# Optimization experiments

Hardware: AMD Instinct MI355X
Metric: run time of the kernel (lower is better)

The kernel has to match this reference:

```python
import jax, jax.numpy as jnp
import numpy as np

N_NODES = 100000
N_EDGES = 1600000
DIM = 64
NUM_HEADS = 4
HEAD_DIM = DIM // NUM_HEADS
QK_SCALE = HEAD_DIM ** -0.5
EPS = 1e-16  # matches torch_geometric softmax denominator eps


def setup_inputs() -> dict:
    key = jax.random.key(0)
    k1, k2, k3 = jax.random.split(key, 3)
    x = jax.random.normal(k1, (N_NODES, DIM), dtype=jnp.float32)
    W_qkv = jax.random.normal(k2, (DIM, 3 * DIM), dtype=jnp.float32) * (DIM ** -0.5)
    b_qkv = jnp.zeros((3 * DIM,), dtype=jnp.float32)
    edge_index = jax.random.randint(k3, (2, N_EDGES), 0, N_NODES, dtype=jnp.int64)
    return {"x": x, "W_qkv": W_qkv, "b_qkv": b_qkv, "edge_index": edge_index}


def reference(x, W_qkv, b_qkv, edge_index):
    N = x.shape[0]
    E = edge_index.shape[1]
    # qkv projection: (N, 3, H, d)
    qkv = (x @ W_qkv + b_qkv).reshape(N, 3, NUM_HEADS, HEAD_DIM)
    s = edge_index[0]  # query (source) node per edge
    t = edge_index[1]  # key/value (target) node per edge
    q = qkv[s, 0] * QK_SCALE  # (E, H, d)
    k = qkv[t, 1]             # (E, H, d)
    v = qkv[t, 2]             # (E, H, d)
    compat = jnp.einsum('ehd,ehd->eh', q, k)  # (E, H)
    # segment softmax keyed by source node (numerically stable)
    m = jax.ops.segment_max(compat, s, num_segments=N)          # (N, H)
    ex = jnp.exp(compat - m[s])                                  # (E, H)
    den = jax.ops.segment_sum(ex, s, num_segments=N)             # (N, H)
    attn = ex / (den[s] + EPS)                                   # (E, H)
    # weighted values, flatten heads, scatter-sum back to source nodes
    msg = (v * attn[..., None]).reshape(E, DIM)                  # (E, dim)
    out = jax.ops.segment_sum(msg, s, num_segments=N)            # (N, dim)
    return out
```

## Files before the change

kernel.cpp:

```cpp
#include <hip/hip_runtime.h>

constexpr int N_NODES = 100000;
constexpr int N_EDGES = 1600000;
constexpr int DIM = 64;
constexpr float QK_SCALE = 0.25f;
constexpr float LOG2E = 1.4426950408889634f;
constexpr float EPS = 1e-16f;

constexpr int NBK = (N_NODES + 255) / 256;
constexpr int BCAP = 8192;
constexpr int SC_CHUNK = 8192;
constexpr int SC_BLOCKS = (N_EDGES + SC_CHUNK - 1) / SC_CHUNK;
constexpr int QK_BLOCKS = (N_NODES + 127) / 128;

typedef __attribute__((ext_vector_type(8))) short short8;
typedef __attribute__((ext_vector_type(4))) float f32x4;

__device__ __forceinline__ unsigned short f32_to_bf16_rne(float f) {
    unsigned int u = __float_as_uint(f);
    u += 0x7fffu + ((u >> 16) & 1u);
    return (unsigned short)(u >> 16);
}
__device__ __forceinline__ float bf_lo(unsigned int u) { return __uint_as_float(u << 16); }
__device__ __forceinline__ float bf_hi(unsigned int u) { return __uint_as_float(u & 0xffff0000u); }

__device__ __forceinline__ float qsum4(float p) {
    int a = __builtin_amdgcn_update_dpp(0, __float_as_int(p), 0xB1, 0xF, 0xF, true);
    p += __int_as_float(a);
    int c = __builtin_amdgcn_update_dpp(0, __float_as_int(p), 0x4E, 0xF, 0xF, true);
    p += __int_as_float(c);
    return p;
}

__device__ __forceinline__ int orig_col(int jp) {
    if (jp < 64) return jp;
    const int p = jp - 64;
    const int chunk = p >> 3, w = p & 7;
    return (w < 4) ? (64 + chunk * 4 + w) : (128 + chunk * 4 + (w - 4));
}

__global__ __launch_bounds__(192) void prep_w(const float* __restrict__ W,
                                              const float* __restrict__ b,
                                              unsigned short* __restrict__ Wbt,
                                              float* __restrict__ bb,
                                              int* __restrict__ bcnt) {
    const int jp = threadIdx.x;
    const int k = blockIdx.x;
    const int oc = orig_col(jp);
    const float sc = (jp < 64) ? QK_SCALE * LOG2E : 1.f;
    Wbt[jp * DIM + k] = f32_to_bf16_rne(W[k * 192 + oc] * sc);
    if (k == 0) {
        bb[jp] = b[oc] * sc;
        for (int i = jp; i < NBK; i += 192) bcnt[i] = 0;
    }
}

__global__ __launch_bounds__(512) void proj_scatter(const float* __restrict__ x,
                                                    const unsigned short* __restrict__ Wbt,
                                                    const float* __restrict__ bb,
                                                    unsigned short* __restrict__ qkv_t,
                                                    const int* __restrict__ ei,
                                                    int* __restrict__ bcnt,
                                                    unsigned int* __restrict__ bbuf) {
    __shared__ int h[NBK];
    __shared__ int lofs[NBK];
    __shared__ int gbase[NBK];
    __shared__ int wsum[8];
    __shared__ unsigned int stage[SC_CHUNK];

    if (blockIdx.x < SC_BLOCKS) {
        const int tid = threadIdx.x;
        const int lane = tid & 63;
        const int wid = tid >> 6;
        const int e0 = blockIdx.x * SC_CHUNK;
        const int n = min(SC_CHUNK, N_EDGES - e0);

        for (int i = tid; i < NBK; i += 512) h[i] = 0;
        __syncthreads();

        for (int i = tid; i < n; i += 512)
            atomicAdd(&h[ei[e0 + i] >> 8], 1);
        __syncthreads();

        const int v = (tid < NBK) ? h[tid] : 0;
        int inc = v;
        #pragma unroll
        for (int d = 1; d < 64; d <<= 1) {
            int u = __shfl_up(inc, d);
            if (lane >= d) inc += u;
        }
        if (lane == 63) wsum[wid] = inc;
        __syncthreads();
        int woff = 0;
        for (int w = 0; w < wid; ++w) woff += wsum[w];
        if (tid < NBK) lofs[tid] = woff + inc - v;
        if (tid < NBK) gbase[tid] = (v > 0) ? atomicAdd(&bcnt[tid], v) : 0;
        __syncthreads();

        for (int i = tid; i < NBK; i += 512) h[i] = 0;
        __syncthreads();

        for (int i = tid; i < n; i += 512) {
            const int s = ei[e0 + i];
            const int t = ei[N_EDGES + e0 + i];
            const int bk = s >> 8;
            const int c = atomicAdd(&h[bk], 1);
            stage[lofs[bk] + c] = (unsigned int)t | ((unsigned int)(s & 255) << 17);
        }
        __syncthreads();

        for (int bk = wid; bk < NBK; bk += 8) {
            const int cnt = h[bk];
            const int lo = lofs[bk];
            unsigned int* dst = bbuf + (size_t)bk * BCAP + gbase[bk];
            for (int i = lane; i < cnt; i += 64) dst[i] = stage[lo + i];
        }
    } else {
        const int lane = threadIdx.x & 63;
        const int wid = threadIdx.x >> 6;
        const int n0 = (blockIdx.x - SC_BLOCKS) * 128 + wid * 16;
        if (n0 >= N_NODES) return;
        const int row = lane & 15;
        const int kg = lane >> 4;

        const int nidx = min(n0 + row, N_NODES - 1);
        const float* xr = x + (size_t)nidx * DIM + kg * 8;
        short8 a0, a1;
        {
            const float4 u0 = *(const float4*)(xr);
            const float4 u1 = *(const float4*)(xr + 4);
            const float4 u2 = *(const float4*)(xr + 32);
            const float4 u3 = *(const float4*)(xr + 36);
            a0[0] = (short)f32_to_bf16_rne(u0.x); a0[1] = (short)f32_to_bf16_rne(u0.y);
            a0[2] = (short)f32_to_bf16_rne(u0.z); a0[3] = (short)f32_to_bf16_rne(u0.w);
            a0[4] = (short)f32_to_bf16_rne(u1.x); a0[5] = (short)f32_to_bf16_rne(u1.y);
            a0[6] = (short)f32_to_bf16_rne(u1.z); a0[7] = (short)f32_to_bf16_rne(u1.w);
            a1[0] = (short)f32_to_bf16_rne(u2.x); a1[1] = (short)f32_to_bf16_rne(u2.y);
            a1[2] = (short)f32_to_bf16_rne(u2.z); a1[3] = (short)f32_to_bf16_rne(u2.w);
            a1[4] = (short)f32_to_bf16_rne(u3.x); a1[5] = (short)f32_to_bf16_rne(u3.y);
            a1[6] = (short)f32_to_bf16_rne(u3.z); a1[7] = (short)f32_to_bf16_rne(u3.w);
        }

        #pragma unroll
        for (int ct = 0; ct < 12; ++ct) {
            const int c0 = ct * 16;
            const float bias = bb[c0 + row];
            f32x4 acc = {bias, bias, bias, bias};
            const short8 b0 = *(const short8*)(Wbt + (c0 + row) * DIM + kg * 8);
            const short8 b1 = *(const short8*)(Wbt + (c0 + row) * DIM + kg * 8 + 32);
            acc = __builtin_amdgcn_mfma_f32_16x16x32_bf16(a0, b0, acc, 0, 0, 0);
            acc = __builtin_amdgcn_mfma_f32_16x16x32_bf16(a1, b1, acc, 0, 0, 0);

            const int colg = c0 + row;
            #pragma unroll
            for (int r = 0; r < 4; ++r) {
                const int node = n0 + kg * 4 + r;
                if (node < N_NODES)
                    qkv_t[(size_t)node * 192 + colg] = f32_to_bf16_rne(acc[r]);
            }
        }
    }
}

__global__ __launch_bounds__(256) void csr_build(const int* __restrict__ bcnt,
                                                 const unsigned int* __restrict__ bbuf,
                                                 int* __restrict__ deg,
                                                 int* __restrict__ off,
                                                 int* __restrict__ sorted_t) {
    __shared__ int h[256];
    __shared__ int lofs[256];
    __shared__ int wsum[4];
    __shared__ int sBase;

    const int tid = threadIdx.x;
    const int lane = tid & 63;
    const int wid = tid >> 6;
    const int bk = blockIdx.x;
    const int n = bcnt[bk];

    int pre = 0;
    for (int i = tid; i < bk; i += 256) pre += bcnt[i];
    #pragma unroll
    for (int d = 1; d < 64; d <<= 1) pre += __shfl_xor(pre, d);
    if (lane == 0) wsum[wid] = pre;
    h[tid] = 0;
    __syncthreads();
    if (tid == 0) sBase = wsum[0] + wsum[1] + wsum[2] + wsum[3];
    __syncthreads();

    const unsigned int* p = bbuf + (size_t)bk * BCAP;
    for (int i = tid; i < n; i += 256)
        atomicAdd(&h[p[i] >> 17], 1);
    __syncthreads();

    const int v = h[tid];
    int inc = v;
    #pragma unroll
    for (int d = 1; d < 64; d <<= 1) {
        int u = __shfl_up(inc, d);
        if (lane >= d) inc += u;
    }
    if (lane == 63) wsum[wid] = inc;
    __syncthreads();
    int woff = 0;
    for (int w = 0; w < wid; ++w) woff += wsum[w];
    const int exc = woff + inc - v;
    lofs[tid] = exc;
    const int node = bk * 256 + tid;
    if (node < N_NODES) { deg[node] = v; off[node] = sBase + exc; }
    __syncthreads();

    h[tid] = 0;
    __syncthreads();
    int* dstbase = sorted_t + sBase;
    for (int i = tid; i < n; i += 256) {
        const unsigned int e = p[i];
        const int s8 = e >> 17;
        const int c = atomicAdd(&h[s8], 1);
        dstbase[lofs[s8] + c] = (int)(e & 0x1FFFFu);
    }
}

__global__ __launch_bounds__(256) void node_pass(const unsigned short* __restrict__ qkv,
                                                 const int* __restrict__ off,
                                                 const int* __restrict__ deg,
                                                 const int* __restrict__ sorted_t,
                                                 float* __restrict__ out) {
    const int node = blockIdx.x * 4 + (threadIdx.x >> 6);
    const int lane = threadIdx.x & 63;
    if (node >= N_NODES) return;
    const int eg = lane >> 4;
    const int q16 = lane & 15;

    const int o = off[node];
    const int d = deg[node];

    const uint2 qu = *(const uint2*)(qkv + (size_t)node * 192 + q16 * 4);
    const float qx = bf_lo(qu.x), qy = bf_hi(qu.x);
    const float qz = bf_lo(qu.y), qw = bf_hi(qu.y);

    const float M0 = -1e30f, MASKV = -2e30f;
    float m = M0;
    float l = 0.f;
    float4 acc = make_float4(0.f, 0.f, 0.f, 0.f);

    for (int j = 0; j < d; j += 16) {
        const int b0 = j + eg * 4;
        const int dm = d - 1;
        const int t0 = sorted_t[o + min(b0,     dm)];
        const int t1 = sorted_t[o + min(b0 + 1, dm)];
        const int t2 = sorted_t[o + min(b0 + 2, dm)];
        const int t3 = sorted_t[o + min(b0 + 3, dm)];
        const uint4 A0 = *(const uint4*)(qkv + (size_t)t0 * 192 + 64 + q16 * 8);
        const uint4 A1 = *(const uint4*)(qkv + (size_t)t1 * 192 + 64 + q16 * 8);
        const uint4 A2 = *(const uint4*)(qkv + (size_t)t2 * 192 + 64 + q16 * 8);
        const uint4 A3 = *(const uint4*)(qkv + (size_t)t3 * 192 + 64 + q16 * 8);
        float p0 = qx * bf_lo(A0.x) + qy * bf_hi(A0.x) + qz * bf_lo(A0.y) + qw * bf_hi(A0.y);
        float p1 = qx * bf_lo(A1.x) + qy * bf_hi(A1.x) + qz * bf_lo(A1.y) + qw * bf_hi(A1.y);
        float p2 = qx * bf_lo(A2.x) + qy * bf_hi(A2.x) + qz * bf_lo(A2.y) + qw * bf_hi(A2.y);
        float p3 = qx * bf_lo(A3.x) + qy * bf_hi(A3.x) + qz * bf_lo(A3.y) + qw * bf_hi(A3.y);
        p0 = qsum4(p0); p1 = qsum4(p1); p2 = qsum4(p2); p3 = qsum4(p3);
        p0 = (b0     < d) ? p0 : MASKV;
        p1 = (b0 + 1 < d) ? p1 : MASKV;
        p2 = (b0 + 2 < d) ? p2 : MASKV;
        p3 = (b0 + 3 < d) ? p3 : MASKV;
        const float pm = fmaxf(fmaxf(p0, p1), fmaxf(p2, p3));
        if (__any(pm > m)) {
            const float nm = fmaxf(m, pm);
            const float sc = exp2f(m - nm);
            l *= sc;
            acc.x *= sc; acc.y *= sc; acc.z *= sc; acc.w *= sc;
            m = nm;
        }
        const float e0 = exp2f(p0 - m);
        const float e1 = exp2f(p1 - m);
        const float e2 = exp2f(p2 - m);
        const float e3 = exp2f(p3 - m);
        l += (e0 + e1) + (e2 + e3);
        acc.x = fmaf(e0, bf_lo(A0.z), fmaf(e1, bf_lo(A1.z),
                fmaf(e2, bf_lo(A2.z), fmaf(e3, bf_lo(A3.z), acc.x))));
        acc.y = fmaf(e0, bf_hi(A0.z), fmaf(e1, bf_hi(A1.z),
                fmaf(e2, bf_hi(A2.z), fmaf(e3, bf_hi(A3.z), acc.y))));
        acc.z = fmaf(e0, bf_lo(A0.w), fmaf(e1, bf_lo(A1.w),
                fmaf(e2, bf_lo(A2.w), fmaf(e3, bf_lo(A3.w), acc.z))));
        acc.w = fmaf(e0, bf_hi(A0.w), fmaf(e1, bf_hi(A1.w),
                fmaf(e2, bf_hi(A2.w), fmaf(e3, bf_hi(A3.w), acc.w))));
    }

    float M = fmaxf(m, __shfl_xor(m, 16));
    M = fmaxf(M, __shfl_xor(M, 32));
    const float s = exp2f(m - M);
    l *= s;
    acc.x *= s; acc.y *= s; acc.z *= s; acc.w *= s;

    l += __shfl_xor(l, 16);  l += __shfl_xor(l, 32);
    acc.x += __shfl_xor(acc.x, 16);  acc.x += __shfl_xor(acc.x, 32);
    acc.y += __shfl_xor(acc.y, 16);  acc.y += __shfl_xor(acc.y, 32);
    acc.z += __shfl_xor(acc.z, 16);  acc.z += __shfl_xor(acc.z, 32);
    acc.w += __shfl_xor(acc.w, 16);  acc.w += __shfl_xor(acc.w, 32);

    if (eg == 0) {
        const float inv = 1.f / (l + EPS);
        float4 r = make_float4(acc.x * inv, acc.y * inv, acc.z * inv, acc.w * inv);
        *(float4*)(out + (size_t)node * DIM + q16 * 4) = r;
    }
}

extern "C" void kernel_launch(void* const* d_in, const int* in_sizes, int n_in,
                              void* d_out, int out_size, void* d_ws, size_t ws_size,
                              hipStream_t stream) {
    const float* x = (const float*)d_in[0];
    const float* W = (const float*)d_in[1];
    const float* b = (const float*)d_in[2];
    const int*   ei = (const int*)d_in[3];
    float* out = (float*)d_out;

    unsigned short* qkv_t = (unsigned short*)d_ws;
    unsigned int* bbuf = (unsigned int*)(qkv_t + (size_t)N_NODES * 192);
    int* sorted_t = (int*)(bbuf + (size_t)NBK * BCAP);
    int* deg      = sorted_t + N_EDGES;
    int* off      = deg + N_NODES;
    int* bcnt     = off + N_NODES;
    unsigned short* Wbt = (unsigned short*)(bcnt + NBK);
    float* bb     = (float*)(Wbt + 192 * DIM);

    prep_w<<<64, 192, 0, stream>>>(W, b, Wbt, bb, bcnt);
    proj_scatter<<<SC_BLOCKS + QK_BLOCKS, 512, 0, stream>>>(x, Wbt, bb, qkv_t, ei, bcnt, bbuf);
    csr_build<<<NBK, 256, 0, stream>>>(bcnt, bbuf, deg, off, sorted_t);
    node_pass<<<(N_NODES + 3) / 4, 256, 0, stream>>>(qkv_t, off, deg, sorted_t, out);
}
```

Before: 128.7 us.

## Fuse CSR build into attention pass using shared-memory sorted targets

Merges the csr_build and node_pass kernels into one csr_attn kernel. Each block handles a quarter of a 256-node bucket: it rebuilds the bucket histogram, scatters only its own 64 nodes' target indices into a shared-memory array, and then runs the online-softmax attention for those nodes. This drops the global sorted_t/deg/off arrays, their write and reread, and one kernel launch. In exchange, every bucket's edges are read and histogrammed four times, each wave walks 16 nodes in sequence, and the fixed ST_CAP of 1536 shared slots can overflow if a 64-node slice has many edges.

```diff
diff --git a/kernel.cpp b/kernel.cpp
--- a/kernel.cpp
+++ b/kernel.cpp
@@ -12,6 +12,7 @@
 constexpr int SC_CHUNK = 8192;
 constexpr int SC_BLOCKS = (N_EDGES + SC_CHUNK - 1) / SC_CHUNK;
 constexpr int QK_BLOCKS = (N_NODES + 127) / 128;
+constexpr int ST_CAP = 1536;
 
 typedef __attribute__((ext_vector_type(8))) short short8;
 typedef __attribute__((ext_vector_type(4))) float f32x4;
@@ -162,33 +163,26 @@
     }
 }
 
-__global__ __launch_bounds__(256) void csr_build(const int* __restrict__ bcnt,
-                                                 const unsigned int* __restrict__ bbuf,
-                                                 int* __restrict__ deg,
-                                                 int* __restrict__ off,
-                                                 int* __restrict__ sorted_t) {
+__global__ __launch_bounds__(256) void csr_attn(const int* __restrict__ bcnt,
+                                                const unsigned int* __restrict__ bbuf,
+                                                const unsigned short* __restrict__ qkv,
+                                                float* __restrict__ out) {
     __shared__ int h[256];
     __shared__ int lofs[256];
+    __shared__ int cur[64];
     __shared__ int wsum[4];
-    __shared__ int sBase;
+    __shared__ int st[ST_CAP];
 
     const int tid = threadIdx.x;
     const int lane = tid & 63;
     const int wid = tid >> 6;
-    const int bk = blockIdx.x;
+    const int bk = blockIdx.x >> 2;
+    const int nl0 = (blockIdx.x & 3) * 64;
     const int n = bcnt[bk];
-
-    int pre = 0;
-    for (int i = tid; i < bk; i += 256) pre += bcnt[i];
-    #pragma unroll
-    for (int d = 1; d < 64; d <<= 1) pre += __shfl_xor(pre, d);
-    if (lane == 0) wsum[wid] = pre;
+    const unsigned int* p = bbuf + (size_t)bk * BCAP;
+
     h[tid] = 0;
     __syncthreads();
-    if (tid == 0) sBase = wsum[0] + wsum[1] + wsum[2] + wsum[3];
-    __syncthreads();
-
-    const unsigned int* p = bbuf + (size_t)bk * BCAP;
     for (int i = tid; i < n; i += 256)
         atomicAdd(&h[p[i] >> 17], 1);
     __syncthreads();
@@ -204,105 +198,102 @@
     __syncthreads();
     int woff = 0;
     for (int w = 0; w < wid; ++w) woff += wsum[w];
-    const int exc = woff + inc - v;
-    lofs[tid] = exc;
-    const int node = bk * 256 + tid;
-    if (node < N_NODES) { deg[node] = v; off[node] = sBase + exc; }
-    __syncthreads();
-
-    h[tid] = 0;
-    __syncthreads();
-    int* dstbase = sorted_t + sBase;
+    lofs[tid] = woff + inc - v;
+    if (tid < 64) cur[tid] = 0;
+    __syncthreads();
+
+    const int base = lofs[nl0];
+
     for (int i = tid; i < n; i += 256) {
         const unsigned int e = p[i];
         const int s8 = e >> 17;
-        const int c = atomicAdd(&h[s8], 1);
-        dstbase[lofs[s8] + c] = (int)(e & 0x1FFFFu);
-    }
-}
-
-__global__ __launch_bounds__(256) void node_pass(const unsigned short* __restrict__ qkv,
-                                                 const int* __restrict__ off,
-                                                 const int* __restrict__ deg,
-                                                 const int* __restrict__ sorted_t,
-                                                 float* __restrict__ out) {
-    const int node = blockIdx.x * 4 + (threadIdx.x >> 6);
-    const int lane = threadIdx.x & 63;
-    if (node >= N_NODES) return;
+        const int r = s8 - nl0;
+        if ((unsigned)r < 64u) {
+            const int c = atomicAdd(&cur[r], 1);
+            st[lofs[s8] - base + c] = (int)(e & 0x1FFFFu);
+        }
+    }
+    __syncthreads();
+
     const int eg = lane >> 4;
     const int q16 = lane & 15;
-
-    const int o = off[node];
-    const int d = deg[node];
-
-    const uint2 qu = *(const uint2*)(qkv + (size_t)node * 192 + q16 * 4);
-    const float qx = bf_lo(qu.x), qy = bf_hi(qu.x);
-    const float qz = bf_lo(qu.y), qw = bf_hi(qu.y);
-
     const float M0 = -1e30f, MASKV = -2e30f;
-    float m = M0;
-    float l = 0.f;
-    float4 acc = make_float4(0.f, 0.f, 0.f, 0.f);
-
-    for (int j = 0; j < d; j += 16) {
-        const int b0 = j + eg * 4;
-        const int dm = d - 1;
-        const int t0 = sorted_t[o + min(b0,     dm)];
-        const int t1 = sorted_t[o + min(b0 + 1, dm)];
-        const int t2 = sorted_t[o + min(b0 + 2, dm)];
-        const int t3 = sorted_t[o + min(b0 + 3, dm)];
-        const uint4 A0 = *(const uint4*)(qkv + (size_t)t0 * 192 + 64 + q16 * 8);
-        const uint4 A1 = *(const uint4*)(qkv + (size_t)t1 * 192 + 64 + q16 * 8);
-        const uint4 A2 = *(const uint4*)(qkv + (size_t)t2 * 192 + 64 + q16 * 8);
-        const uint4 A3 = *(const uint4*)(qkv + (size_t)t3 * 192 + 64 + q16 * 8);
-        float p0 = qx * bf_lo(A0.x) + qy * bf_hi(A0.x) + qz * bf_lo(A0.y) + qw * bf_hi(A0.y);
-        float p1 = qx * bf_lo(A1.x) + qy * bf_hi(A1.x) + qz * bf_lo(A1.y) + qw * bf_hi(A1.y);
-        float p2 = qx * bf_lo(A2.x) + qy * bf_hi(A2.x) + qz * bf_lo(A2.y) + qw * bf_hi(A2.y);
-        float p3 = qx * bf_lo(A3.x) + qy * bf_hi(A3.x) + qz * bf_lo(A3.y) + qw * bf_hi(A3.y);
-        p0 = qsum4(p0); p1 = qsum4(p1); p2 = qsum4(p2); p3 = qsum4(p3);
-        p0 = (b0     < d) ? p0 : MASKV;
-        p1 = (b0 + 1 < d) ? p1 : MASKV;
-        p2 = (b0 + 2 < d) ? p2 : MASKV;
-        p3 = (b0 + 3 < d) ? p3 : MASKV;
-        const float pm = fmaxf(fmaxf(p0, p1), fmaxf(p2, p3));
-        if (__any(pm > m)) {
-            const float nm = fmaxf(m, pm);
-            const float sc = exp2f(m - nm);
-            l *= sc;
-            acc.x *= sc; acc.y *= sc; acc.z *= sc; acc.w *= sc;
-            m = nm;
-        }
-        const float e0 = exp2f(p0 - m);
-        const float e1 = exp2f(p1 - m);
-        const float e2 = exp2f(p2 - m);
-        const float e3 = exp2f(p3 - m);
-        l += (e0 + e1) + (e2 + e3);
-        acc.x = fmaf(e0, bf_lo(A0.z), fmaf(e1, bf_lo(A1.z),
-                fmaf(e2, bf_lo(A2.z), fmaf(e3, bf_lo(A3.z), acc.x))));
-        acc.y = fmaf(e0, bf_hi(A0.z), fmaf(e1, bf_hi(A1.z),
-                fmaf(e2, bf_hi(A2.z), fmaf(e3, bf_hi(A3.z), acc.y))));
-        acc.z = fmaf(e0, bf_lo(A0.w), fmaf(e1, bf_lo(A1.w),
-                fmaf(e2, bf_lo(A2.w), fmaf(e3, bf_lo(A3.w), acc.z))));
-        acc.w = fmaf(e0, bf_hi(A0.w), fmaf(e1, bf_hi(A1.w),
-                fmaf(e2, bf_hi(A2.w), fmaf(e3, bf_hi(A3.w), acc.w))));
-    }
-
-    float M = fmaxf(m, __shfl_xor(m, 16));
-    M = fmaxf(M, __shfl_xor(M, 32));
-    const float s = exp2f(m - M);
-    l *= s;
-    acc.x *= s; acc.y *= s; acc.z *= s; acc.w *= s;
-
-    l += __shfl_xor(l, 16);  l += __shfl_xor(l, 32);
-    acc.x += __shfl_xor(acc.x, 16);  acc.x += __shfl_xor(acc.x, 32);
-    acc.y += __shfl_xor(acc.y, 16);  acc.y += __shfl_xor(acc.y, 32);
-    acc.z += __shfl_xor(acc.z, 16);  acc.z += __shfl_xor(acc.z, 32);
-    acc.w += __shfl_xor(acc.w, 16);  acc.w += __shfl_xor(acc.w, 32);
-
-    if (eg == 0) {
-        const float inv = 1.f / (l + EPS);
-        float4 r = make_float4(acc.x * inv, acc.y * inv, acc.z * inv, acc.w * inv);
-        *(float4*)(out + (size_t)node * DIM + q16 * 4) = r;
+
+    for (int r = 0; r < 16; ++r) {
+        const int nl = nl0 + wid * 16 + r;
+        const int node = bk * 256 + nl;
+        if (node >= N_NODES) break;
+        const int o = lofs[nl] - base;
+        const int d = cur[nl - nl0];
+
+        const uint2 qu = *(const uint2*)(qkv + (size_t)node * 192 + q16 * 4);
+        const float qx = bf_lo(qu.x), qy = bf_hi(qu.x);
+        const float qz = bf_lo(qu.y), qw = bf_hi(qu.y);
+
+        float m = M0;
+        float l = 0.f;
+        float4 acc = make_float4(0.f, 0.f, 0.f, 0.f);
+        const int dm = (d > 0) ? d - 1 : 0;
+
+        for (int j = 0; j < d; j += 16) {
+            const int b0 = j + eg * 4;
+            const int t0 = st[o + min(b0,     dm)];
+            const int t1 = st[o + min(b0 + 1, dm)];
+            const int t2 = st[o + min(b0 + 2, dm)];
+            const int t3 = st[o + min(b0 + 3, dm)];
+            const uint4 A0 = *(const uint4*)(qkv + (size_t)t0 * 192 + 64 + q16 * 8);
+            const uint4 A1 = *(const uint4*)(qkv + (size_t)t1 * 192 + 64 + q16 * 8);
+            const uint4 A2 = *(const uint4*)(qkv + (size_t)t2 * 192 + 64 + q16 * 8);
+            const uint4 A3 = *(const uint4*)(qkv + (size_t)t3 * 192 + 64 + q16 * 8);
+            float p0 = qx * bf_lo(A0.x) + qy * bf_hi(A0.x) + qz * bf_lo(A0.y) + qw * bf_hi(A0.y);
+            float p1 = qx * bf_lo(A1.x) + qy * bf_hi(A1.x) + qz * bf_lo(A1.y) + qw * bf_hi(A1.y);
+            float p2 = qx * bf_lo(A2.x) + qy * bf_hi(A2.x) + qz * bf_lo(A2.y) + qw * bf_hi(A2.y);
+            float p3 = qx * bf_lo(A3.x) + qy * bf_hi(A3.x) + qz * bf_lo(A3.y) + qw * bf_hi(A3.y);
+            p0 = qsum4(p0); p1 = qsum4(p1); p2 = qsum4(p2); p3 = qsum4(p3);
+            p0 = (b0     < d) ? p0 : MASKV;
+            p1 = (b0 + 1 < d) ? p1 : MASKV;
+            p2 = (b0 + 2 < d) ? p2 : MASKV;
+            p3 = (b0 + 3 < d) ? p3 : MASKV;
+            const float pm = fmaxf(fmaxf(p0, p1), fmaxf(p2, p3));
+            if (__any(pm > m)) {
+                const float nm = fmaxf(m, pm);
+                const float sc = exp2f(m - nm);
+                l *= sc;
+                acc.x *= sc; acc.y *= sc; acc.z *= sc; acc.w *= sc;
+                m = nm;
+            }
+            const float e0 = exp2f(p0 - m);
+            const float e1 = exp2f(p1 - m);
+            const float e2 = exp2f(p2 - m);
+            const float e3 = exp2f(p3 - m);
+            l += (e0 + e1) + (e2 + e3);
+            acc.x = fmaf(e0, bf_lo(A0.z), fmaf(e1, bf_lo(A1.z),
+                    fmaf(e2, bf_lo(A2.z), fmaf(e3, bf_lo(A3.z), acc.x))));
+            acc.y = fmaf(e0, bf_hi(A0.z), fmaf(e1, bf_hi(A1.z),
+                    fmaf(e2, bf_hi(A2.z), fmaf(e3, bf_hi(A3.z), acc.y))));
+            acc.z = fmaf(e0, bf_lo(A0.w), fmaf(e1, bf_lo(A1.w),
+                    fmaf(e2, bf_lo(A2.w), fmaf(e3, bf_lo(A3.w), acc.z))));
+            acc.w = fmaf(e0, bf_hi(A0.w), fmaf(e1, bf_hi(A1.w),
+                    fmaf(e2, bf_hi(A2.w), fmaf(e3, bf_hi(A3.w), acc.w))));
+        }
+
+        float M = fmaxf(m, __shfl_xor(m, 16));
+        M = fmaxf(M, __shfl_xor(M, 32));
+        const float s = exp2f(m - M);
+        l *= s;
+        acc.x *= s; acc.y *= s; acc.z *= s; acc.w *= s;
+
+        l += __shfl_xor(l, 16);  l += __shfl_xor(l, 32);
+        acc.x += __shfl_xor(acc.x, 16);  acc.x += __shfl_xor(acc.x, 32);
+        acc.y += __shfl_xor(acc.y, 16);  acc.y += __shfl_xor(acc.y, 32);
+        acc.z += __shfl_xor(acc.z, 16);  acc.z += __shfl_xor(acc.z, 32);
+        acc.w += __shfl_xor(acc.w, 16);  acc.w += __shfl_xor(acc.w, 32);
+
+        if (eg == 0) {
+            const float inv = 1.f / (l + EPS);
+            float4 rv = make_float4(acc.x * inv, acc.y * inv, acc.z * inv, acc.w * inv);
+            *(float4*)(out + (size_t)node * DIM + q16 * 4) = rv;
+        }
     }
 }
 
@@ -317,15 +308,11 @@
 
     unsigned short* qkv_t = (unsigned short*)d_ws;
     unsigned int* bbuf = (unsigned int*)(qkv_t + (size_t)N_NODES * 192);
-    int* sorted_t = (int*)(bbuf + (size_t)NBK * BCAP);
-    int* deg      = sorted_t + N_EDGES;
-    int* off      = deg + N_NODES;
-    int* bcnt     = off + N_NODES;
+    int* bcnt = (int*)(bbuf + (size_t)NBK * BCAP);
     unsigned short* Wbt = (unsigned short*)(bcnt + NBK);
-    float* bb     = (float*)(Wbt + 192 * DIM);
+    float* bb = (float*)(Wbt + 192 * DIM);
 
     prep_w<<<64, 192, 0, stream>>>(W, b, Wbt, bb, bcnt);
     proj_scatter<<<SC_BLOCKS + QK_BLOCKS, 512, 0, stream>>>(x, Wbt, bb, qkv_t, ei, bcnt, bbuf);
-    csr_build<<<NBK, 256, 0, stream>>>(bcnt, bbuf, deg, off, sorted_t);
-    node_pass<<<(N_NODES + 3) / 4, 256, 0, stream>>>(qkv_t, off, deg, sorted_t, out);
-}
+    csr_attn<<<NBK * 4, 256, 0, stream>>>(bcnt, bbuf, qkv_t, out);
+}
```

Result: slower. 134.3 us (+4.4%).
